# Kernel tuning notes

Hardware: AMD Instinct MI355X
Metric: run time of the kernel (lower is better)

Reference implementation:

```python
import math
import jax, jax.numpy as jnp
from jax import lax
import numpy as np

B, M, L = 256, 21, 512
P, S, D = 16, 8, 256
NL, EXP, H, LAM = 3, 2, 96, 0.01
T = (L - P) // S + 1  # 63 patches
HID = D * EXP


def _pos_enc():
    pe = np.zeros((T, D), np.float32)
    pos = np.arange(T, dtype=np.float32)[:, None]
    div = np.exp(np.arange(0, D, 2, dtype=np.float32) * (-math.log(10000.0) / D))
    pe[:, 0::2] = np.sin(pos * div)
    pe[:, 1::2] = np.cos(pos * div)
    return jnp.asarray(pe)


def _clin(zr, zi, Wr, Wi, br, bi):
    # faithful to torch: bias br added to both terms of yr (cancels), bi added twice in yi
    yr = (zr @ Wr.T + br) - (zi @ Wi.T + br)
    yi = (zr @ Wi.T + bi) + (zi @ Wr.T + bi)
    return yr, yi


def _softshrink(zr, zi):
    mag = jnp.sqrt(zr * zr + zi * zi)
    scale = jnp.maximum(mag - LAM, 0.0) / (mag + 1e-8) * (mag > LAM).astype(zr.dtype)
    return zr * scale, zi * scale


def _layernorm(x, g, b):
    mu = jnp.mean(x, -1, keepdims=True)
    var = jnp.mean((x - mu) ** 2, -1, keepdims=True)
    return (x - mu) / jnp.sqrt(var + 1e-5) * g + b


def _block(x, p):
    (Tw, Tb, Gew, Geb, Gpw, Gpb,
     H1Wr, H1Wi, H1br, H1bi, H2Wr, H2Wi, H2br, H2bi, lng, lnb) = p
    g = jax.nn.gelu(x @ Gew.T + Geb, approximate=False) @ Gpw.T + Gpb
    zf = jnp.fft.rfft(x, axis=1)  # FFT along time/patch axis T
    zr, zi = zf.real, zf.imag
    zr, zi = _clin(zr, zi, H1Wr, H1Wi, H1br, H1bi)
    zr, zi = _softshrink(zr, zi)
    zr, zi = _clin(zr, zi, H2Wr, H2Wi, H2br, H2bi)
    pt = jnp.fft.irfft(lax.complex(zr, zi), n=x.shape[1], axis=1)
    out = (g * pt) @ Tw.T + Tb
    return _layernorm(out + x, lng, lnb)


def _forward(x, conv_w, conv_b, tp, sp, gate_w, gate_b, proj_w, proj_b):
    # per-instance, per-variable norm over time (biased std, eps on std)
    mean = jnp.mean(x, -1, keepdims=True)
    std = jnp.sqrt(jnp.mean((x - mean) ** 2, -1, keepdims=True))
    xn = (x - mean) / (std + 1e-5)
    patches = lax.conv_general_dilated(xn, conv_w, (S,), 'VALID',
                                       dimension_numbers=('NCH', 'OIH', 'NCH'))
    patches = patches + conv_b[None, :, None]
    h = patches.transpose(0, 2, 1) + _pos_enc()[None]  # (B, T, D)
    t = h
    s = h
    for i in range(NL):
        t = _block(t, tuple(a[i] for a in tp))
        s = _block(s, tuple(a[i] for a in sp))
    gate = jax.nn.sigmoid(t @ gate_w.T + gate_b)
    feat = gate * t + (1.0 - gate) * s
    out = feat.reshape(feat.shape[0], -1) @ proj_w.T + proj_b
    y = out.reshape(-1, M, H) * (std + 1e-5) + mean
    return y


def setup_inputs() -> dict:
    key = jax.random.key(0)
    ks = iter(jax.random.split(key, 64))

    def nrm(shape, scale):
        return jax.random.normal(next(ks), shape, jnp.float32) * scale

    inp = {'x': nrm((B, M, L), 1.0)}
    inp['conv_w'] = nrm((D, M, P), 1.0 / math.sqrt(M * P))
    inp['conv_b'] = jnp.zeros((D,), jnp.float32)

    def layer_params(prefix):
        d = {}
        d[prefix + 'Tw'] = nrm((NL, D, D), 1.0 / math.sqrt(D))
        d[prefix + 'Tb'] = jnp.zeros((NL, D), jnp.float32)
        d[prefix + 'Gew'] = nrm((NL, HID, D), 1.0 / math.sqrt(D))
        d[prefix + 'Geb'] = jnp.zeros((NL, HID), jnp.float32)
        d[prefix + 'Gpw'] = nrm((NL, D, HID), 1.0 / math.sqrt(HID))
        d[prefix + 'Gpb'] = jnp.zeros((NL, D), jnp.float32)
        for hname in ('H1', 'H2'):
            d[prefix + hname + 'Wr'] = nrm((NL, D, D), 1.0 / math.sqrt(D))
            d[prefix + hname + 'Wi'] = nrm((NL, D, D), 1.0 / math.sqrt(D))
            d[prefix + hname + 'br'] = jnp.zeros((NL, D), jnp.float32)
            d[prefix + hname + 'bi'] = jnp.zeros((NL, D), jnp.float32)
        d[prefix + 'lng'] = jnp.ones((NL, D), jnp.float32)
        d[prefix + 'lnb'] = jnp.zeros((NL, D), jnp.float32)
        return d

    inp.update(layer_params('t_'))
    inp.update(layer_params('s_'))
    inp['gate_w'] = nrm((1, D), 1.0 / math.sqrt(D))
    inp['gate_b'] = jnp.zeros((1,), jnp.float32)
    inp['proj_w'] = nrm((M * H, T * D), 1.0 / math.sqrt(T * D))
    inp['proj_b'] = jnp.zeros((M * H,), jnp.float32)
    return inp


def reference(x, conv_w, conv_b,
              t_Tw, t_Tb, t_Gew, t_Geb, t_Gpw, t_Gpb,
              t_H1Wr, t_H1Wi, t_H1br, t_H1bi, t_H2Wr, t_H2Wi, t_H2br, t_H2bi, t_lng, t_lnb,
              s_Tw, s_Tb, s_Gew, s_Geb, s_Gpw, s_Gpb,
              s_H1Wr, s_H1Wi, s_H1br, s_H1bi, s_H2Wr, s_H2Wi, s_H2br, s_H2bi, s_lng, s_lnb,
              gate_w, gate_b, proj_w, proj_b):
    tp = (t_Tw, t_Tb, t_Gew, t_Geb, t_Gpw, t_Gpb,
          t_H1Wr, t_H1Wi, t_H1br, t_H1bi, t_H2Wr, t_H2Wi, t_H2br, t_H2bi, t_lng, t_lnb)
    sp = (s_Tw, s_Tb, s_Gew, s_Geb, s_Gpw, s_Gpb,
          s_H1Wr, s_H1Wi, s_H1br, s_H1bi, s_H2Wr, s_H2Wi, s_H2br, s_H2bi, s_lng, s_lnb)
    return _forward(x, conv_w, conv_b, tp, sp, gate_w, gate_b, proj_w, proj_b)
```

## Files before the change

kernel.cpp:

```cpp
#include <hip/hip_runtime.h>
#include <cstddef>
#include <cstdint>

#define B_    256
#define M_    21
#define L_    512
#define D_    256
#define T_    63
#define F_    32
#define NT_   16128
#define HID_  512
#define KCP_  352
#define H_    96
#define LAM_  0.01f
#define PZ_   16

typedef __attribute__((ext_vector_type(8))) short short8;
typedef __attribute__((ext_vector_type(4))) float f32x4;
typedef unsigned int u32;
typedef const u32 __attribute__((address_space(1)))* gas1_t;
typedef u32 __attribute__((address_space(3)))* las3_t;

__device__ __forceinline__ void async_copy16(const void* g, void* l) {
  __builtin_amdgcn_global_load_lds((gas1_t)g, (las3_t)(uintptr_t)l, 16, 0, 0);
}
__device__ __forceinline__ unsigned short f2bf(float x) {
  unsigned u = __float_as_uint(x);
  return (unsigned short)((u + 0x7FFF + ((u >> 16) & 1)) >> 16);
}
__device__ __forceinline__ float bf2f(unsigned short u) {
  return __uint_as_float(((unsigned)u) << 16);
}
__device__ __forceinline__ float gelu_exact(float v) {
  return 0.5f * v * (1.0f + erff(v * 0.70710678118654752f));
}
__device__ __forceinline__ float block_sum256(float v, float* red4) {
  #pragma unroll
  for (int off = 32; off > 0; off >>= 1) v += __shfl_down(v, off, 64);
  if ((threadIdx.x & 63) == 0) red4[threadIdx.x >> 6] = v;
  __syncthreads();
  float r = red4[0] + red4[1] + red4[2] + red4[3];
  __syncthreads();
  return r;
}
__device__ __forceinline__ float wave_sum(float v) {
  #pragma unroll
  for (int off = 1; off < 64; off <<= 1) v += __shfl_xor(v, off, 64);
  return v;
}

struct CvtEnt { const float* src; unsigned short* dst; int rows, scol, dcol, blk0; };
struct CvtArgs { CvtEnt e[19]; int nent; };
__global__ __launch_bounds__(256) void wprep_kernel(CvtArgs a) {
  int blk = blockIdx.x, e = 0;
  while (e + 1 < a.nent && a.e[e + 1].blk0 <= blk) ++e;
  CvtEnt en = a.e[e];
  int idx = (blk - en.blk0) * 256 + threadIdx.x;
  int total = en.rows * en.dcol;
  if (idx >= total) return;
  int r = idx / en.dcol, c = idx - r * en.dcol;
  float v = (c < en.scol) ? en.src[(size_t)r * en.scol + c] : 0.f;
  en.dst[idx] = f2bf(v);
}

struct CatArgs { const float* wr[12]; const float* wi[12]; };
__global__ __launch_bounds__(256) void wcat_kernel(CatArgs a, unsigned short* dst) {
  int e = blockIdx.x >> 10;
  int idx = ((blockIdx.x & 1023) << 8) + threadIdx.x;
  int r = idx >> 9, c = idx & 511;
  int cp = r >> 1, p = r & 1, d = c >> 1, q = c & 1;
  const float* wr = a.wr[e];
  const float* wi = a.wi[e];
  float v;
  if (p == 0) v = (q == 0) ? wr[cp * 256 + d] : -wi[cp * 256 + d];
  else        v = (q == 0) ? wi[cp * 256 + d] :  wr[cp * 256 + d];
  dst[(size_t)e * 262144 + idx] = f2bf(v);
}

template <int ACT, int OUTBF, int BIASM, int KSTEPS, int CVTA, int CVTW,
          int SHRINK, int MULPT, int SPLITK, int BK, int RT>
__global__ __launch_bounds__(256) void mm_kernel(
    const void* __restrict__ Av,
    const unsigned short* __restrict__ W0, const unsigned short* __restrict__ W1,
    const float* __restrict__ Wf,
    const float* __restrict__ b0, const float* __restrict__ b1,
    const unsigned short* __restrict__ ptb,
    void* __restrict__ Cv,
    const int K, const int Dout, const int ksteps_rt, const int yhalf,
    const int prow, const int totk) {
  constexpr int NP = BK / 32;
  constexpr int RWS = 32 * RT;
  __shared__ __align__(16) unsigned short As[NP * RWS * 32];
  __shared__ __align__(16) unsigned short Bs[NP * 128 * 32];
  const int tid = threadIdx.x, w = tid >> 6, lane = tid & 63;
  const int quad = lane >> 4, r16 = lane & 15;
  int nks = KSTEPS ? KSTEPS : ksteps_rt;
  const int ksbeg = SPLITK ? (int)blockIdx.z * nks : 0;
  if (SPLITK) { int rem = totk - ksbeg; if (nks > rem) nks = rem; }
  const int kst = ksbeg * BK;
  const int tower = ((int)blockIdx.y >= yhalf) ? 1 : 0;
  const unsigned short* Wb = tower ? W1 : W0;
  const float* bias = tower ? b1 : b0;

  const unsigned short* Ab = (const unsigned short*)Av;
  const float* Af = (const float*)Av;
  const unsigned short* gA = nullptr;
  unsigned short* lA = As + (w * 8 * RT) * 32;
  if (!CVTA) gA = Ab + (size_t)((int)blockIdx.y * RWS + w * 8 * RT + (lane >> 2)) * K
                     + kst + (lane & 3) * 8;
  const unsigned short* gB = nullptr;
  unsigned short* lB = Bs + (w * 32) * 32;
  if (!CVTW) gB = Wb + (size_t)((int)blockIdx.x * 128 + w * 32 + (lane >> 2)) * K
                     + kst + (lane & 3) * 8;
  const int crow = tid >> 3;
  const int ck4  = (tid & 7) << 2;

  float4 areg[NP][RT];
  float4 wreg[NP][4];
  auto loadA = [&](int ksi) {
    #pragma unroll
    for (int p = 0; p < NP; ++p)
      #pragma unroll
      for (int rr = 0; rr < RT; ++rr)
        areg[p][rr] = *reinterpret_cast<const float4*>(
            Af + (size_t)((int)blockIdx.y * RWS + crow + 32 * rr) * K
               + kst + ksi * BK + p * 32 + ck4);
  };
  auto loadW = [&](int ksi) {
    #pragma unroll
    for (int p = 0; p < NP; ++p)
      #pragma unroll
      for (int rr = 0; rr < 4; ++rr) {
        int wrow = (int)blockIdx.x * 128 + crow + 32 * rr;
        if (wrow >= Dout) wrow = Dout - 1;
        wreg[p][rr] = *reinterpret_cast<const float4*>(
            Wf + (size_t)wrow * K + kst + ksi * BK + p * 32 + ck4);
      }
  };
  if (CVTA) loadA(0);
  if (CVTW) loadW(0);

  f32x4 acc[RT][4];
  #pragma unroll
  for (int i = 0; i < RT; ++i)
    #pragma unroll
    for (int j = 0; j < 4; ++j)
      #pragma unroll
      for (int r = 0; r < 4; ++r) acc[i][j][r] = 0.f;

  for (int ks = 0; ks < nks; ++ks) {
    if (!CVTA) {
      #pragma unroll
      for (int p = 0; p < NP; ++p)
        #pragma unroll
        for (int c = 0; c < RT / 2; ++c)
          async_copy16(gA + (size_t)(c * 16) * K + p * 32,
                       lA + p * (RWS * 32) + c * 16 * 32);
      gA += BK;
    } else {
      #pragma unroll
      for (int p = 0; p < NP; ++p)
        #pragma unroll
        for (int rr = 0; rr < RT; ++rr) {
          float4 v = areg[p][rr];
          ushort4 o; o.x = f2bf(v.x); o.y = f2bf(v.y); o.z = f2bf(v.z); o.w = f2bf(v.w);
          *reinterpret_cast<ushort4*>(As + p * (RWS * 32) + (crow + 32 * rr) * 32 + ck4) = o;
        }
    }
    if (!CVTW) {
      #pragma unroll
      for (int p = 0; p < NP; ++p) {
        async_copy16(gB + p * 32, lB + p * 4096);
        async_copy16(gB + (size_t)16 * K + p * 32, lB + p * 4096 + 16 * 32);
      }
      gB += BK;
    } else {
      #pragma unroll
      for (int p = 0; p < NP; ++p)
        #pragma unroll
        for (int rr = 0; rr < 4; ++rr) {
          float4 v = wreg[p][rr];
          ushort4 o; o.x = f2bf(v.x); o.y = f2bf(v.y); o.z = f2bf(v.z); o.w = f2bf(v.w);
          *reinterpret_cast<ushort4*>(Bs + p * 4096 + (crow + 32 * rr) * 32 + ck4) = o;
        }
    }
    __syncthreads();
    if (CVTA && ks + 1 < nks) loadA(ks + 1);
    if (CVTW && ks + 1 < nks) loadW(ks + 1);
    #pragma unroll
    for (int p = 0; p < NP; ++p) {
      const unsigned short* pa = As + p * (RWS * 32) + ((w >> 1) * 16 * RT + r16) * 32 + quad * 8;
      const unsigned short* pb = Bs + p * 4096 + (64 * (w & 1) + r16) * 32 + quad * 8;
      short8 af[RT], bfv[4];
      #pragma unroll
      for (int i = 0; i < RT; ++i) af[i] = *reinterpret_cast<const short8*>(pa + i * 512);
      #pragma unroll
      for (int j = 0; j < 4; ++j) bfv[j] = *reinterpret_cast<const short8*>(pb + j * 512);
      #pragma unroll
      for (int i = 0; i < RT; ++i)
        #pragma unroll
        for (int j = 0; j < 4; ++j)
          acc[i][j] = __builtin_amdgcn_mfma_f32_16x16x32_bf16(af[i], bfv[j], acc[i][j], 0, 0, 0);
    }
    __syncthreads();
  }

  float* Cf = (float*)Cv;
  unsigned short* Cb = (unsigned short*)Cv;
  if (SPLITK) Cf += (size_t)blockIdx.z * prow * Dout;
  const int colb = (int)blockIdx.x * 128 + 64 * (w & 1) + r16;
  const int rowb = (int)blockIdx.y * RWS + 16 * RT * (w >> 1) + quad * 4;
  #pragma unroll
  for (int j = 0; j < 4; ++j) {
    int col = colb + 16 * j;
    float bv = 0.f;
    if (BIASM == 0) bv = bias[col];
    else if (BIASM == 1) bv = (col & 1) ? 2.0f * bias[col >> 1] : 0.f;
    bool colok = (BIASM != 2) || (col < Dout);
    #pragma unroll
    for (int i = 0; i < RT; ++i) {
      #pragma unroll
      for (int r = 0; r < 4; ++r) {
        int row = rowb + 16 * i + r;
        float v = acc[i][j][r] + bv;
        if (ACT == 1) v = gelu_exact(v);
        if (SHRINK) {
          float o = __shfl_xor(v, 1, 64);
          float mag = sqrtf(v * v + o * o);
          float s = (mag > LAM_) ? (mag - LAM_) / (mag + 1e-8f) : 0.f;
          v *= s;
        }
        if (MULPT) v *= bf2f(ptb[(size_t)row * Dout + col]);
        if (colok) {
          if (OUTBF) Cb[(size_t)row * Dout + col] = f2bf(v);
          else       Cf[(size_t)row * Dout + col] = v;
        }
      }
    }
  }
}

__global__ __launch_bounds__(256) void norm_kernel(const float* __restrict__ x,
    float* __restrict__ xn, float* __restrict__ meanb, float* __restrict__ stdb) {
  __shared__ float red[4];
  int bm = blockIdx.x;
  const float* xr = x + (size_t)bm * L_;
  float v0 = xr[threadIdx.x], v1 = xr[threadIdx.x + 256];
  float mu = block_sum256(v0 + v1, red) * (1.0f / L_);
  float d0 = v0 - mu, d1 = v1 - mu;
  float sd = sqrtf(block_sum256(d0 * d0 + d1 * d1, red) * (1.0f / L_));
  float inv = 1.0f / (sd + 1e-5f);
  float* xo = xn + (size_t)bm * L_;
  xo[threadIdx.x] = d0 * inv;
  xo[threadIdx.x + 256] = d1 * inv;
  if (threadIdx.x == 0) { meanb[bm] = mu; stdb[bm] = sd; }
}

__global__ __launch_bounds__(256) void im2col_kernel(const float* __restrict__ xn,
                                                     unsigned short* __restrict__ im) {
  int row = blockIdx.x;
  int b = row / T_, t = row - b * T_;
  const float* xb = xn + (size_t)b * M_ * L_ + t * 8;
  unsigned short* o = im + (size_t)row * KCP_;
  for (int i = threadIdx.x; i < KCP_; i += 256) {
    float v = 0.f;
    if (i < 336) { int m = i >> 4, p = i & 15; v = xb[m * L_ + p]; }
    o[i] = f2bf(v);
  }
}

__global__ __launch_bounds__(256) void add_pe_kernel(const float* __restrict__ g0,
                                                     float* __restrict__ x32) {
  int row = blockIdx.x, d = threadIdx.x;
  int t = row % T_;
  size_t idx = (size_t)row * D_ + d;
  float freq = expf((float)(d & ~1) * (-9.210340371976184f / 256.0f));
  float ang = (float)t * freq;
  float pe = (d & 1) ? cosf(ang) : sinf(ang);
  float h = g0[idx] + pe;
  x32[idx] = h;
  x32[idx + (size_t)NT_ * D_] = h;
}

__global__ __launch_bounds__(256) void dft_kernel(const float* __restrict__ X,
                                                  unsigned short* __restrict__ Zcat) {
  __shared__ float2 tw[T_ * F_];
  int bt = blockIdx.x, d = threadIdx.x;
  for (int i = threadIdx.x; i < T_ * F_; i += 256) {
    int t = i >> 5, f = i & 31;
    int k = (f * t) % T_;
    float sn, cs;
    sincosf((6.283185307179586f / 63.0f) * (float)k, &sn, &cs);
    tw[i] = make_float2(cs, -sn);
  }
  __syncthreads();
  const float* xb = X + (size_t)bt * T_ * D_ + d;
  float ar[F_], ai[F_];
  #pragma unroll
  for (int f = 0; f < F_; ++f) { ar[f] = 0.f; ai[f] = 0.f; }
  for (int t = 0; t < T_; ++t) {
    float v = xb[(size_t)t * D_];
    const float2* w = &tw[t * F_];
    #pragma unroll
    for (int f = 0; f < F_; ++f) {
      float2 c = w[f];
      ar[f] = fmaf(v, c.x, ar[f]);
      ai[f] = fmaf(v, c.y, ai[f]);
    }
  }
  u32* z = reinterpret_cast<u32*>(Zcat + (size_t)bt * F_ * 512);
  #pragma unroll
  for (int f = 0; f < F_; ++f)
    z[f * 256 + d] = (u32)f2bf(ar[f]) | ((u32)f2bf(ai[f]) << 16);
}

__global__ __launch_bounds__(256) void irfft_kernel(const unsigned short* __restrict__ Y,
                                                    unsigned short* __restrict__ ptb) {
  __shared__ float2 tw[T_ * 31];
  int bt = blockIdx.x, d = threadIdx.x;
  for (int i = threadIdx.x; i < T_ * 31; i += 256) {
    int t = i / 31, f = i - t * 31 + 1;
    int k = (f * t) % T_;
    float sn, cs;
    sincosf((6.283185307179586f / 63.0f) * (float)k, &sn, &cs);
    tw[i] = make_float2(cs * (2.0f / 63.0f), -sn * (2.0f / 63.0f));
  }
  __syncthreads();
  const unsigned short* yb = Y + (size_t)bt * F_ * 512 + 2 * d;
  float y0 = bf2f(yb[0]) * (1.0f / 63.0f);
  float yr[31], yi[31];
  #pragma unroll
  for (int f = 1; f < F_; ++f) {
    u32 p = *reinterpret_cast<const u32*>(yb + (size_t)f * 512);
    yr[f - 1] = bf2f((unsigned short)(p & 0xffff));
    yi[f - 1] = bf2f((unsigned short)(p >> 16));
  }
  unsigned short* po = ptb + (size_t)bt * T_ * D_ + d;
  for (int t = 0; t < T_; ++t) {
    const float2* w = &tw[t * 31];
    float acc0 = y0, acc1 = 0.f;
    #pragma unroll
    for (int f = 0; f < 31; f += 2) {
      float2 c = w[f];
      acc0 = fmaf(yr[f], c.x, fmaf(yi[f], c.y, acc0));
      if (f + 1 < 31) {
        float2 c1 = w[f + 1];
        acc1 = fmaf(yr[f + 1], c1.x, fmaf(yi[f + 1], c1.y, acc1));
      }
    }
    po[(size_t)t * D_] = f2bf(acc0 + acc1);
  }
}

__global__ __launch_bounds__(256) void ln_kernel(const float* __restrict__ outb,
    float* __restrict__ x, const float* __restrict__ g0, const float* __restrict__ b0,
    const float* __restrict__ g1, const float* __restrict__ b1, int yhalf) {
  int row = blockIdx.x * 4 + (threadIdx.x >> 6);
  int lane = threadIdx.x & 63;
  const float* g = (row >= yhalf) ? g1 : g0;
  const float* b = (row >= yhalf) ? b1 : b0;
  size_t base = (size_t)row * D_ + lane * 4;
  float4 ov = *reinterpret_cast<const float4*>(outb + base);
  float4 xv = *reinterpret_cast<const float4*>(x + base);
  float v0 = ov.x + xv.x, v1 = ov.y + xv.y, v2 = ov.z + xv.z, v3 = ov.w + xv.w;
  float mu = wave_sum(v0 + v1 + v2 + v3) * (1.0f / D_);
  v0 -= mu; v1 -= mu; v2 -= mu; v3 -= mu;
  float var = wave_sum(v0 * v0 + v1 * v1 + v2 * v2 + v3 * v3) * (1.0f / D_);
  float is = rsqrtf(var + 1e-5f);
  float4 gv = *reinterpret_cast<const float4*>(g + lane * 4);
  float4 bv = *reinterpret_cast<const float4*>(b + lane * 4);
  float4 o;
  o.x = v0 * is * gv.x + bv.x;
  o.y = v1 * is * gv.y + bv.y;
  o.z = v2 * is * gv.z + bv.z;
  o.w = v3 * is * gv.w + bv.w;
  *reinterpret_cast<float4*>(x + base) = o;
}

__global__ __launch_bounds__(256) void gate_feat_kernel(const float* __restrict__ x32,
    const float* __restrict__ gw, const float* __restrict__ gb,
    unsigned short* __restrict__ featbf) {
  int row = blockIdx.x * 4 + (threadIdx.x >> 6);
  int lane = threadIdx.x & 63;
  size_t base = (size_t)row * D_ + lane * 4;
  float4 tv = *reinterpret_cast<const float4*>(x32 + base);
  float4 sv = *reinterpret_cast<const float4*>(x32 + base + (size_t)NT_ * D_);
  float4 gv = *reinterpret_cast<const float4*>(gw + lane * 4);
  float dot = wave_sum(tv.x * gv.x + tv.y * gv.y + tv.z * gv.z + tv.w * gv.w) + gb[0];
  float gate = 1.0f / (1.0f + expf(-dot));
  ushort4 o;
  o.x = f2bf(gate * tv.x + (1.0f - gate) * sv.x);
  o.y = f2bf(gate * tv.y + (1.0f - gate) * sv.y);
  o.z = f2bf(gate * tv.z + (1.0f - gate) * sv.z);
  o.w = f2bf(gate * tv.w + (1.0f - gate) * sv.w);
  *reinterpret_cast<ushort4*>(featbf + base) = o;
}

__global__ __launch_bounds__(256) void final_kernel(const float* __restrict__ part,
    const float* __restrict__ pb, const float* __restrict__ stdb,
    const float* __restrict__ meanb, float* __restrict__ y) {
  int i = blockIdx.x * 256 + threadIdx.x;
  float acc = 0.f;
  #pragma unroll
  for (int z = 0; z < PZ_; ++z) acc += part[(size_t)z * 516096 + i];
  int b = i / 2016;
  int col = i - b * 2016;
  int m = col / H_;
  float sc = stdb[b * M_ + m] + 1e-5f;
  y[i] = (acc + pb[col]) * sc + meanb[b * M_ + m];
}

extern "C" void kernel_launch(void* const* d_in, const int* in_sizes, int n_in,
                              void* d_out, int out_size, void* d_ws, size_t ws_size,
                              hipStream_t stream) {
  const float* x      = (const float*)d_in[0];
  const float* conv_w = (const float*)d_in[1];
  const float* conv_b = (const float*)d_in[2];
  const float* tP[16];
  const float* sP[16];
  for (int i = 0; i < 16; ++i) tP[i] = (const float*)d_in[3 + i];
  for (int i = 0; i < 16; ++i) sP[i] = (const float*)d_in[19 + i];
  const float* gate_w = (const float*)d_in[35];
  const float* gate_b = (const float*)d_in[36];
  const float* proj_w = (const float*)d_in[37];
  const float* proj_b = (const float*)d_in[38];
  float* out = (float*)d_out;

  float* ws    = (float*)d_ws;
  float* x32   = ws;
  unsigned short* wb = (unsigned short*)(x32 + 8257536);
  float* meanb = x32 + 8257536 + 2600960;
  float* stdb  = meanb + 5376;
  float* R1    = stdb + 5376 + 16;
  float* R2    = R1 + 8388608;

  unsigned short* im2colB = (unsigned short*)R1;
  unsigned short* Zcat    = (unsigned short*)R1;
  unsigned short* Ycat1   = (unsigned short*)(R1 + 4194304);
  unsigned short* ptb     = (unsigned short*)(R1 + 4194304);
  unsigned short* gp      = (unsigned short*)R1;
  unsigned short* featbf  = (unsigned short*)R1;

  float* xn     = R2;
  float* g0buf  = R2;
  unsigned short* Ycat2b = (unsigned short*)R2;
  unsigned short* hidB = (unsigned short*)R2;
  float* outb   = R2;
  float* part   = R2;

  unsigned short* convW = wb;
  unsigned short* sets  = wb + 90112;
  unsigned short* catW  = wb + 90112 + 1966080;

  CvtArgs ca; int blk0 = 0, ne = 0;
  auto add_ent = [&](const float* s, unsigned short* d, int rows, int scol, int dcol) {
    ca.e[ne].src = s; ca.e[ne].dst = d; ca.e[ne].rows = rows;
    ca.e[ne].scol = scol; ca.e[ne].dcol = dcol; ca.e[ne].blk0 = blk0;
    blk0 += (rows * dcol + 255) / 256; ++ne;
  };
  add_ent(conv_w, convW, 256, 336, 352);
  for (int tw = 0; tw < 2; ++tw) {
    const float** Pp = tw ? (const float**)sP : (const float**)tP;
    for (int l = 0; l < 3; ++l) {
      unsigned short* sb = sets + (size_t)(tw * 3 + l) * 327680;
      add_ent(Pp[2] + (size_t)l * 131072, sb,          512, 256, 256);
      add_ent(Pp[4] + (size_t)l * 131072, sb + 131072, 256, 512, 512);
      add_ent(Pp[0] + (size_t)l * 65536,  sb + 262144, 256, 256, 256);
    }
  }
  ca.nent = ne;
  wprep_kernel<<<blk0, 256, 0, stream>>>(ca);

  CatArgs cat;
  for (int tw = 0; tw < 2; ++tw) {
    const float** Pp = tw ? (const float**)sP : (const float**)tP;
    for (int l = 0; l < 3; ++l) {
      int e0 = (tw * 3 + l) * 2;
      cat.wr[e0]     = Pp[6]  + (size_t)l * 65536;
      cat.wi[e0]     = Pp[7]  + (size_t)l * 65536;
      cat.wr[e0 + 1] = Pp[10] + (size_t)l * 65536;
      cat.wi[e0 + 1] = Pp[11] + (size_t)l * 65536;
    }
  }
  wcat_kernel<<<12 * 1024, 256, 0, stream>>>(cat, catW);

  norm_kernel<<<B_ * M_, 256, 0, stream>>>(x, xn, meanb, stdb);
  im2col_kernel<<<NT_, 256, 0, stream>>>(xn, im2colB);
  mm_kernel<0, 0, 0, 11, 0, 0, 0, 0, 0, 32, 2><<<dim3(2, 252), 256, 0, stream>>>(
      im2colB, convW, convW, nullptr, conv_b, conv_b, nullptr, g0buf,
      KCP_, 256, 0, 1 << 30, 0, 0);
  add_pe_kernel<<<NT_, 256, 0, stream>>>(g0buf, x32);

  for (int l = 0; l < 3; ++l) {
    unsigned short* st0 = sets + (size_t)l * 327680;
    unsigned short* st1 = sets + (size_t)(3 + l) * 327680;
    unsigned short* c1t0 = catW + (size_t)((0 + l) * 2) * 262144;
    unsigned short* c2t0 = c1t0 + 262144;
    unsigned short* c1t1 = catW + (size_t)((3 + l) * 2) * 262144;
    unsigned short* c2t1 = c1t1 + 262144;

    dft_kernel<<<2 * B_, 256, 0, stream>>>(x32, Zcat);
    mm_kernel<0, 1, 1, 8, 0, 0, 1, 0, 0, 64, 2><<<dim3(4, 256), 256, 0, stream>>>(
        Zcat, c1t0, c1t1, nullptr, tP[9] + (size_t)l * D_, sP[9] + (size_t)l * D_,
        nullptr, Ycat1, 512, 512, 0, 128, 0, 0);
    mm_kernel<0, 1, 1, 8, 0, 0, 0, 0, 0, 64, 2><<<dim3(4, 256), 256, 0, stream>>>(
        Ycat1, c2t0, c2t1, nullptr, tP[13] + (size_t)l * D_, sP[13] + (size_t)l * D_,
        nullptr, Ycat2b, 512, 512, 0, 128, 0, 0);
    irfft_kernel<<<2 * B_, 256, 0, stream>>>(Ycat2b, ptb);
    mm_kernel<1, 1, 0, 4, 1, 0, 0, 0, 0, 64, 2><<<dim3(4, 504), 256, 0, stream>>>(
        x32, st0, st1, nullptr, tP[3] + (size_t)l * HID_, sP[3] + (size_t)l * HID_,
        nullptr, hidB, 256, 512, 0, 252, 0, 0);
    mm_kernel<0, 1, 0, 8, 0, 0, 0, 1, 0, 64, 2><<<dim3(2, 504), 256, 0, stream>>>(
        hidB, st0 + 131072, st1 + 131072, nullptr,
        tP[5] + (size_t)l * D_, sP[5] + (size_t)l * D_, ptb, gp, 512, 256, 0, 252, 0, 0);
    mm_kernel<0, 0, 0, 4, 0, 0, 0, 0, 0, 64, 2><<<dim3(2, 504), 256, 0, stream>>>(
        gp, st0 + 262144, st1 + 262144, nullptr,
        tP[1] + (size_t)l * D_, sP[1] + (size_t)l * D_, nullptr, outb, 256, 256, 0, 252, 0, 0);
    ln_kernel<<<2 * NT_ / 4, 256, 0, stream>>>(outb, x32,
        tP[14] + (size_t)l * D_, tP[15] + (size_t)l * D_,
        sP[14] + (size_t)l * D_, sP[15] + (size_t)l * D_, NT_);
  }

  gate_feat_kernel<<<NT_ / 4, 256, 0, stream>>>(x32, gate_w, gate_b, featbf);
  mm_kernel<0, 0, 2, 0, 0, 1, 0, 0, 1, 32, 2><<<dim3(16, 4, PZ_), 256, 0, stream>>>(
      featbf, nullptr, nullptr, proj_w, nullptr, nullptr, nullptr, part,
      NT_, 2016, 32, 1 << 30, 256, 504);
  final_kernel<<<2016, 256, 0, stream>>>(part, proj_b, stdb, meanb, out);
}
```

Measured before the change: 1.010 ms.

## Double-buffer register prefetch in GEMM and add register-staged A path for projection

The GEMM kernel's register-staged loads become double-buffered: two k-steps are prefetched ahead through alternating register sets, so global latency is hidden across more compute. A new CVTA==2 mode loads bf16 A tiles through registers instead of async LDS copies, and the final projection GEMM uses it. Split-K depth rises from 16 to 24 with fewer k-steps per slice, and the partial buffer moves to a separate region. The cost is higher register pressure, which may lower occupancy, plus more partial sums for the final reduction.

```diff
diff --git a/kernel.cpp b/kernel.cpp
--- a/kernel.cpp
+++ b/kernel.cpp
@@ -13,7 +13,7 @@
 #define KCP_  352
 #define H_    96
 #define LAM_  0.01f
-#define PZ_   16
+#define PZ_   24
 
 typedef __attribute__((ext_vector_type(8))) short short8;
 typedef __attribute__((ext_vector_type(4))) float f32x4;
@@ -106,8 +106,8 @@
   const float* Af = (const float*)Av;
   const unsigned short* gA = nullptr;
   unsigned short* lA = As + (w * 8 * RT) * 32;
-  if (!CVTA) gA = Ab + (size_t)((int)blockIdx.y * RWS + w * 8 * RT + (lane >> 2)) * K
-                     + kst + (lane & 3) * 8;
+  if (CVTA != 1) gA = Ab + (size_t)((int)blockIdx.y * RWS + w * 8 * RT + (lane >> 2)) * K
+                      + kst + (lane & 3) * 8;
   const unsigned short* gB = nullptr;
   unsigned short* lB = Bs + (w * 32) * 32;
   if (!CVTW) gB = Wb + (size_t)((int)blockIdx.x * 128 + w * 32 + (lane >> 2)) * K
@@ -115,30 +115,39 @@
   const int crow = tid >> 3;
   const int ck4  = (tid & 7) << 2;
 
-  float4 areg[NP][RT];
-  float4 wreg[NP][4];
-  auto loadA = [&](int ksi) {
+  float4 aregA[NP][RT], aregB[NP][RT];
+  float4 wregA[NP][4],  wregB[NP][4];
+  auto loadA = [&](int ksi, float4 (&dst)[NP][RT]) {
     #pragma unroll
     for (int p = 0; p < NP; ++p)
       #pragma unroll
       for (int rr = 0; rr < RT; ++rr)
-        areg[p][rr] = *reinterpret_cast<const float4*>(
+        dst[p][rr] = *reinterpret_cast<const float4*>(
             Af + (size_t)((int)blockIdx.y * RWS + crow + 32 * rr) * K
                + kst + ksi * BK + p * 32 + ck4);
   };
-  auto loadW = [&](int ksi) {
+  auto loadA2 = [&](int ksi, float4 (&dst)[NP][RT]) {
+    #pragma unroll
+    for (int p = 0; p < NP; ++p)
+      #pragma unroll
+      for (int c = 0; c < RT / 2; ++c)
+        dst[p][c] = *reinterpret_cast<const float4*>(
+            gA + (size_t)(c * 16) * K + ksi * BK + p * 32);
+  };
+  auto loadW = [&](int ksi, float4 (&dst)[NP][4]) {
     #pragma unroll
     for (int p = 0; p < NP; ++p)
       #pragma unroll
       for (int rr = 0; rr < 4; ++rr) {
         int wrow = (int)blockIdx.x * 128 + crow + 32 * rr;
         if (wrow >= Dout) wrow = Dout - 1;
-        wreg[p][rr] = *reinterpret_cast<const float4*>(
+        dst[p][rr] = *reinterpret_cast<const float4*>(
             Wf + (size_t)wrow * K + kst + ksi * BK + p * 32 + ck4);
       }
   };
-  if (CVTA) loadA(0);
-  if (CVTW) loadW(0);
+  if (CVTA == 1) { loadA(0, aregA);  if (nks > 1) loadA(1, aregB); }
+  if (CVTA == 2) { loadA2(0, aregA); if (nks > 1) loadA2(1, aregB); }
+  if (CVTW)      { loadW(0, wregA);  if (nks > 1) loadW(1, wregB); }
 
   f32x4 acc[RT][4];
   #pragma unroll
@@ -148,8 +157,8 @@
       #pragma unroll
       for (int r = 0; r < 4; ++r) acc[i][j][r] = 0.f;
 
-  for (int ks = 0; ks < nks; ++ks) {
-    if (!CVTA) {
+  auto kstep = [&](int ks, float4 (&ar)[NP][RT], float4 (&wr)[NP][4]) {
+    if (CVTA == 0) {
       #pragma unroll
       for (int p = 0; p < NP; ++p)
         #pragma unroll
@@ -157,15 +166,21 @@
           async_copy16(gA + (size_t)(c * 16) * K + p * 32,
                        lA + p * (RWS * 32) + c * 16 * 32);
       gA += BK;
-    } else {
+    } else if (CVTA == 1) {
       #pragma unroll
       for (int p = 0; p < NP; ++p)
         #pragma unroll
         for (int rr = 0; rr < RT; ++rr) {
-          float4 v = areg[p][rr];
+          float4 v = ar[p][rr];
           ushort4 o; o.x = f2bf(v.x); o.y = f2bf(v.y); o.z = f2bf(v.z); o.w = f2bf(v.w);
           *reinterpret_cast<ushort4*>(As + p * (RWS * 32) + (crow + 32 * rr) * 32 + ck4) = o;
         }
+    } else {
+      #pragma unroll
+      for (int p = 0; p < NP; ++p)
+        #pragma unroll
+        for (int c = 0; c < RT / 2; ++c)
+          *reinterpret_cast<float4*>(lA + p * (RWS * 32) + c * 16 * 32 + lane * 8) = ar[p][c];
     }
     if (!CVTW) {
       #pragma unroll
@@ -179,14 +194,15 @@
       for (int p = 0; p < NP; ++p)
         #pragma unroll
         for (int rr = 0; rr < 4; ++rr) {
-          float4 v = wreg[p][rr];
+          float4 v = wr[p][rr];
           ushort4 o; o.x = f2bf(v.x); o.y = f2bf(v.y); o.z = f2bf(v.z); o.w = f2bf(v.w);
           *reinterpret_cast<ushort4*>(Bs + p * 4096 + (crow + 32 * rr) * 32 + ck4) = o;
         }
     }
     __syncthreads();
-    if (CVTA && ks + 1 < nks) loadA(ks + 1);
-    if (CVTW && ks + 1 < nks) loadW(ks + 1);
+    if (CVTA == 1 && ks + 2 < nks) loadA(ks + 2, ar);
+    if (CVTA == 2 && ks + 2 < nks) loadA2(ks + 2, ar);
+    if (CVTW && ks + 2 < nks) loadW(ks + 2, wr);
     #pragma unroll
     for (int p = 0; p < NP; ++p) {
       const unsigned short* pa = As + p * (RWS * 32) + ((w >> 1) * 16 * RT + r16) * 32 + quad * 8;
@@ -203,6 +219,15 @@
           acc[i][j] = __builtin_amdgcn_mfma_f32_16x16x32_bf16(af[i], bfv[j], acc[i][j], 0, 0, 0);
     }
     __syncthreads();
+  };
+
+  if (CVTA == 0 && !CVTW) {
+    for (int ks = 0; ks < nks; ++ks) kstep(ks, aregA, wregA);
+  } else {
+    for (int ks = 0; ks < nks; ks += 2) {
+      kstep(ks, aregA, wregA);
+      if (ks + 1 < nks) kstep(ks + 1, aregB, wregB);
+    }
   }
 
   float* Cf = (float*)Cv;
@@ -446,7 +471,7 @@
   unsigned short* Ycat2b = (unsigned short*)R2;
   unsigned short* hidB = (unsigned short*)R2;
   float* outb   = R2;
-  float* part   = R2;
+  float* part   = R1 + 2064384;
 
   unsigned short* convW = wb;
   unsigned short* sets  = wb + 90112;
@@ -522,8 +547,8 @@
   }
 
   gate_feat_kernel<<<NT_ / 4, 256, 0, stream>>>(x32, gate_w, gate_b, featbf);
-  mm_kernel<0, 0, 2, 0, 0, 1, 0, 0, 1, 32, 2><<<dim3(16, 4, PZ_), 256, 0, stream>>>(
+  mm_kernel<0, 0, 2, 0, 2, 1, 0, 0, 1, 32, 2><<<dim3(16, 4, PZ_), 256, 0, stream>>>(
       featbf, nullptr, nullptr, proj_w, nullptr, nullptr, nullptr, part,
-      NT_, 2016, 32, 1 << 30, 256, 504);
+      NT_, 2016, 21, 1 << 30, 256, 504);
   final_kernel<<<2016, 256, 0, stream>>>(part, proj_b, stdb, meanb, out);
 }
```

New measurement: 1.062 ms. 5.1% more time.
